# Kernel optimization log

Hardware: AMD Instinct MI355X
Metric: run time of the kernel (lower is better)

The kernel has to match this reference:

```python
import jax, jax.numpy as jnp
import numpy as np

B, T, U = 2048, 200, 128


def setup_inputs() -> dict:
    key = jax.random.key(0)
    ks = jax.random.split(key, 9)
    s = 1.0 / np.sqrt(U)
    inp = {
        "interest_states": jax.random.normal(ks[0], (B, T, U), dtype=jnp.float32),
        "attention_scores": jax.random.uniform(ks[1], (B, T, 1), dtype=jnp.float32),
        "W_xu": jax.random.normal(ks[2], (U, U), dtype=jnp.float32) * s,
        "b_xu": jnp.zeros((U,), dtype=jnp.float32),
        "W_hu": jax.random.normal(ks[3], (U, U), dtype=jnp.float32) * s,
        "b_hu": jnp.zeros((U,), dtype=jnp.float32),
        "W_xr": jax.random.normal(ks[4], (U, U), dtype=jnp.float32) * s,
        "b_xr": jnp.zeros((U,), dtype=jnp.float32),
        "W_hr": jax.random.normal(ks[5], (U, U), dtype=jnp.float32) * s,
        "b_hr": jnp.zeros((U,), dtype=jnp.float32),
        "W_xc": jax.random.normal(ks[6], (U, U), dtype=jnp.float32) * s,
        "b_xc": jnp.zeros((U,), dtype=jnp.float32),
        "W_hc": jax.random.normal(ks[7], (U, U), dtype=jnp.float32) * s,
        "b_hc": jnp.zeros((U,), dtype=jnp.float32),
    }
    return inp


def reference(interest_states, attention_scores, W_xu, b_xu, W_hu, b_hu,
              W_xr, b_xr, W_hr, b_hr, W_xc, b_xc, W_hc, b_hc):
    # Precompute input-side projections for all timesteps (batched GEMMs).
    xu = jnp.einsum('btu,uv->btv', interest_states, W_xu) + b_xu  # [B,T,U]
    xr = jnp.einsum('btu,uv->btv', interest_states, W_xr) + b_xr
    xc = jnp.einsum('btu,uv->btv', interest_states, W_xc) + b_xc
    # Time-major for scan: [T,B,U] / [T,B,1]
    xu_t = jnp.swapaxes(xu, 0, 1)
    xr_t = jnp.swapaxes(xr, 0, 1)
    xc_t = jnp.swapaxes(xc, 0, 1)
    att_t = jnp.swapaxes(attention_scores, 0, 1)  # [T,B,1]

    def step(h, inp):
        xu_i, xr_i, xc_i, a_i = inp
        u = jax.nn.sigmoid(xu_i + h @ W_hu + b_hu)       # update gate [B,U]
        r = jax.nn.sigmoid(xr_i + h @ W_hr + b_hr)       # reset gate  [B,U]
        c = jnp.tanh(xc_i + (r * h) @ W_hc + b_hc)       # candidate   [B,U]
        au = a_i * u                                     # attention-scaled update gate
        h_new = (1.0 - au) * h + au * c
        return h_new, None

    h0 = jnp.zeros((interest_states.shape[0], W_hu.shape[0]), dtype=interest_states.dtype)
    h_final, _ = jax.lax.scan(step, h0, (xu_t, xr_t, xc_t, att_t))
    return h_final  # [B,U]
```

## Files before the change

kernel.cpp:

```cpp
#include <hip/hip_runtime.h>
#include <hip/hip_bf16.h>

#define B_  2048
#define T_  200
#define U_  128
#define NB  8
#define PITCH 136

typedef __attribute__((ext_vector_type(8))) short short8;
typedef __attribute__((ext_vector_type(4))) float f32x4;
typedef __attribute__((ext_vector_type(2))) float f32x2;
typedef __attribute__((ext_vector_type(2))) unsigned uint2v;

static __device__ inline float sigm_pre(float sum, float bS) {
  float e = __builtin_amdgcn_exp2f(fmaf(sum, -1.44269504088896340736f, bS));
  return __builtin_amdgcn_rcpf(1.0f + e);
}
static __device__ inline float tanh_pre(float sum, float bS) {
  float e = __builtin_amdgcn_exp2f(fmaf(sum, 2.88539008177792681472f, bS));
  float r = __builtin_amdgcn_rcpf(1.0f + e);
  return fmaf(-2.0f, r, 1.0f);
}
static __device__ inline unsigned pk2(float a, float b) {
  union { __hip_bfloat162 h; unsigned u; } c;
  float2 t; t.x = a; t.y = b;
  c.h = __float22bfloat162_rn(t);
  return c.u;
}
static __device__ inline short f2bf(float f) {
  union { float f; unsigned u; } v; v.f = f;
  unsigned r = v.u + 0x7FFFu + ((v.u >> 16) & 1u);
  return (short)(r >> 16);
}

#define TRFRAG(dst, addr, O0, O1)                                              \
  {                                                                            \
    uint2v _ta, _tb;                                                           \
    asm volatile("ds_read_b64_tr_b16 %0, %1 offset:" O0 : "=v"(_ta) : "v"(addr)); \
    asm volatile("ds_read_b64_tr_b16 %0, %1 offset:" O1 : "=v"(_tb) : "v"(addr)); \
    union { struct { uint2v a, b; } p; short8 s; } _u;                         \
    _u.p.a = _ta; _u.p.b = _tb;                                                \
    dst = _u.s;                                                                \
  }
#define LGKM_WAIT()                                                            \
  asm volatile("s_waitcnt lgkmcnt(0)" ::: "memory");                           \
  __builtin_amdgcn_sched_barrier(0)

__global__ void prep_weights(const float* __restrict__ Wxu, const float* __restrict__ Wxr,
                             const float* __restrict__ Wxc, const float* __restrict__ Whu,
                             const float* __restrict__ Whr, const float* __restrict__ Whc,
                             short* __restrict__ out) {
  const int m = blockIdx.x >> 7;
  const int k = blockIdx.x & 127;
  const int n = threadIdx.x;
  const float* Wp;
  switch (m) {
    case 0: Wp = Wxu; break; case 1: Wp = Wxr; break; case 2: Wp = Wxc; break;
    case 3: Wp = Whu; break; case 4: Wp = Whr; break; default: Wp = Whc; break;
  }
  out[(m * 128 + n) * 128 + k] = f2bf(Wp[k * 128 + n]);
}

__global__ __launch_bounds__(512, 2) void augru_scan(
    const float* __restrict__ IS, const float* __restrict__ ATT,
    const float* __restrict__ bxu, const float* __restrict__ bhu,
    const float* __restrict__ bxr, const float* __restrict__ bhr,
    const float* __restrict__ bxc, const float* __restrict__ bhc,
    const short* __restrict__ WT, float* __restrict__ out) {
  __shared__ __align__(128) short h_T[128][16];
  __shared__ __align__(128) short rh_T[128][16];
  __shared__ __align__(16)  short x_bf[16][PITCH];
  __shared__ __align__(16)  float att_s[T_][NB];

  const int tid  = threadIdx.x;
  const int w    = tid >> 6;
  const int l    = tid & 63;
  const int l15  = l & 15;
  const int lg   = l >> 4;
  const int b0   = blockIdx.x * NB;
  const int col  = w * 16 + l15;

  for (int i = tid; i < (128 * 16 * 2 + 16 * PITCH) / 2; i += 512) {
    if (i < 128 * 16 / 2)               ((int*)h_T)[i] = 0;
    else if (i < 128 * 16)              ((int*)rh_T)[i - 128 * 16 / 2] = 0;
    else                                ((int*)x_bf)[i - 128 * 16] = 0;
  }
  for (int i = tid; i < T_ * NB; i += 512) {
    int r = i / T_, t = i % T_;
    att_s[t][r] = ATT[(size_t)(b0 + r) * T_ + t];
  }
  const int prow = w;
  const int pc2  = (tid & 63) * 2;
  const float* xptr = IS + (size_t)(b0 + prow) * T_ * U_ + pc2;
  {
    f32x2 xv = *(const f32x2*)xptr;
    *(unsigned*)&x_bf[prow][pc2] = pk2(xv[0], xv[1]);
  }
  short8 Wf[6][4];
#pragma unroll
  for (int m = 0; m < 6; ++m)
#pragma unroll
    for (int kf = 0; kf < 4; ++kf)
      Wf[m][kf] = *(const short8*)(WT + ((m * 128 + col) * 128 + kf * 32 + lg * 8));
#pragma unroll
  for (int m = 0; m < 6; ++m)
#pragma unroll
    for (int kf = 0; kf < 4; ++kf) asm volatile("" : "+v"(Wf[m][kf]));

  const float buS = (bxu[col] + bhu[col]) * -1.44269504088896340736f;
  const float brS = (bxr[col] + bhr[col]) * -1.44269504088896340736f;
  const float bcS = (bxc[col] + bhc[col]) * 2.88539008177792681472f;

  const unsigned trv   = (unsigned)(lg * 256 + l15 * 8);
  const unsigned adr_h = (unsigned)(size_t)(&h_T[0][0]) + trv;
  const unsigned adr_r = (unsigned)(size_t)(&rh_T[0][0]) + trv;

  const f32x4 fz = {0.0f, 0.0f, 0.0f, 0.0f};
  f32x4 hreg = fz;
  float ureg[4];

  for (int t = 0; t < T_; ++t) {
    __syncthreads();
    __builtin_amdgcn_sched_barrier(0);
    short8 ha[4], xa[4];
    TRFRAG(ha[0], adr_h, "0",    "128");
    TRFRAG(ha[1], adr_h, "1024", "1152");
    TRFRAG(ha[2], adr_h, "2048", "2176");
    TRFRAG(ha[3], adr_h, "3072", "3200");
#pragma unroll
    for (int kf = 0; kf < 4; ++kf)
      xa[kf] = *(const short8*)&x_bf[l15][kf * 32 + lg * 8];
    const f32x2 xnext = *(const f32x2*)(xptr + (t < T_ - 1 ? (size_t)(t + 1) * U_ : (size_t)t * U_));
    LGKM_WAIT();

    f32x4 axu = fz, axr = fz, axc = fz, ahu = fz, ahr = fz;
#pragma unroll
    for (int kf = 0; kf < 4; ++kf) {
      axu = __builtin_amdgcn_mfma_f32_16x16x32_bf16(xa[kf], Wf[0][kf], axu, 0, 0, 0);
      axr = __builtin_amdgcn_mfma_f32_16x16x32_bf16(xa[kf], Wf[1][kf], axr, 0, 0, 0);
      axc = __builtin_amdgcn_mfma_f32_16x16x32_bf16(xa[kf], Wf[2][kf], axc, 0, 0, 0);
      ahu = __builtin_amdgcn_mfma_f32_16x16x32_bf16(ha[kf], Wf[3][kf], ahu, 0, 0, 0);
      ahr = __builtin_amdgcn_mfma_f32_16x16x32_bf16(ha[kf], Wf[4][kf], ahr, 0, 0, 0);
    }
    float rh[4];
#pragma unroll
    for (int rg = 0; rg < 4; ++rg) {
      ureg[rg] = sigm_pre(axu[rg] + ahu[rg], buS);
      float rr = sigm_pre(axr[rg] + ahr[rg], brS);
      rh[rg]   = rr * hreg[rg];
    }
    {
      uint2v wv; wv[0] = pk2(rh[0], rh[1]); wv[1] = pk2(rh[2], rh[3]);
      *(uint2v*)&rh_T[col][lg * 4] = wv;
    }
    __syncthreads();
    __builtin_amdgcn_sched_barrier(0);
    short8 ra[4];
    TRFRAG(ra[0], adr_r, "0",    "128");
    TRFRAG(ra[1], adr_r, "1024", "1152");
    TRFRAG(ra[2], adr_r, "2048", "2176");
    TRFRAG(ra[3], adr_r, "3072", "3200");
    const f32x4 a4 = *(const f32x4*)&att_s[t][(lg & 1) * 4];
    LGKM_WAIT();

    f32x4 ahc0 = fz, ahc1 = fz;
    ahc0 = __builtin_amdgcn_mfma_f32_16x16x32_bf16(ra[0], Wf[5][0], ahc0, 0, 0, 0);
    ahc1 = __builtin_amdgcn_mfma_f32_16x16x32_bf16(ra[2], Wf[5][2], ahc1, 0, 0, 0);
    ahc0 = __builtin_amdgcn_mfma_f32_16x16x32_bf16(ra[1], Wf[5][1], ahc0, 0, 0, 0);
    ahc1 = __builtin_amdgcn_mfma_f32_16x16x32_bf16(ra[3], Wf[5][3], ahc1, 0, 0, 0);

    float hv[4];
#pragma unroll
    for (int rg = 0; rg < 4; ++rg) {
      float cc = tanh_pre((axc[rg] + ahc0[rg]) + ahc1[rg], bcS);
      float au = a4[rg] * ureg[rg];
      hv[rg] = fmaf(au, cc - hreg[rg], hreg[rg]);
      hreg[rg] = hv[rg];
    }
    {
      uint2v wv; wv[0] = pk2(hv[0], hv[1]); wv[1] = pk2(hv[2], hv[3]);
      *(uint2v*)&h_T[col][lg * 4] = wv;
    }
    *(unsigned*)&x_bf[prow][pc2] = pk2(xnext[0], xnext[1]);
  }
#pragma unroll
  for (int rg = 0; rg < 4; ++rg) {
    const int row = lg * 4 + rg;
    if (row < NB) out[(size_t)(b0 + row) * U_ + col] = hreg[rg];
  }
}

extern "C" void kernel_launch(void* const* d_in, const int* in_sizes, int n_in,
                              void* d_out, int out_size, void* d_ws, size_t ws_size,
                              hipStream_t stream) {
  const float* IS  = (const float*)d_in[0];
  const float* ATT = (const float*)d_in[1];
  const float* Wxu = (const float*)d_in[2];  const float* bxu = (const float*)d_in[3];
  const float* Whu = (const float*)d_in[4];  const float* bhu = (const float*)d_in[5];
  const float* Wxr = (const float*)d_in[6];  const float* bxr = (const float*)d_in[7];
  const float* Whr = (const float*)d_in[8];  const float* bhr = (const float*)d_in[9];
  const float* Wxc = (const float*)d_in[10]; const float* bxc = (const float*)d_in[11];
  const float* Whc = (const float*)d_in[12]; const float* bhc = (const float*)d_in[13];
  short* WT  = (short*)d_ws;
  float* OUT = (float*)d_out;

  prep_weights<<<dim3(6 * 128), dim3(128), 0, stream>>>(Wxu, Wxr, Wxc, Whu, Whr, Whc, WT);
  augru_scan<<<dim3(B_ / NB), dim3(512), 0, stream>>>(IS, ATT, bxu, bhu, bxr, bhr, bxc, bhc, WT, OUT);
}
```

Measured before the change: 449.2 us.

## Load x fragments directly from global and precompute next-step input projections

Removes the x_bf shared-memory staging buffer: each lane now loads its own fp32 x fragment from global memory, converts it to bf16 in registers, and runs the input-side MFMAs for step t+1 at the end of step t. This takes the x projections off the critical path between the first barrier and the gate activations. The hidden-side MFMAs are split into two accumulator chains to shorten dependency latency, and two sched_barriers are dropped. The cost is more global load traffic, since rows are duplicated across lanes (l15&7), plus extra register pressure from the prefetched xraw and the carried accumulators.

Result: slower. 747.2 us (+66.3%).

```diff
diff --git a/kernel.cpp b/kernel.cpp
--- a/kernel.cpp
+++ b/kernel.cpp
@@ -5,11 +5,9 @@
 #define T_  200
 #define U_  128
 #define NB  8
-#define PITCH 136
 
 typedef __attribute__((ext_vector_type(8))) short short8;
 typedef __attribute__((ext_vector_type(4))) float f32x4;
-typedef __attribute__((ext_vector_type(2))) float f32x2;
 typedef __attribute__((ext_vector_type(2))) unsigned uint2v;
 
 static __device__ inline float sigm_pre(float sum, float bS) {
@@ -31,6 +29,12 @@
   union { float f; unsigned u; } v; v.f = f;
   unsigned r = v.u + 0x7FFFu + ((v.u >> 16) & 1u);
   return (short)(r >> 16);
+}
+static __device__ inline short8 cvt8(const f32x4 a, const f32x4 b) {
+  union { unsigned u[4]; short8 s; } c;
+  c.u[0] = pk2(a[0], a[1]); c.u[1] = pk2(a[2], a[3]);
+  c.u[2] = pk2(b[0], b[1]); c.u[3] = pk2(b[2], b[3]);
+  return c.s;
 }
 
 #define TRFRAG(dst, addr, O0, O1)                                              \
@@ -69,7 +73,6 @@
     const short* __restrict__ WT, float* __restrict__ out) {
   __shared__ __align__(128) short h_T[128][16];
   __shared__ __align__(128) short rh_T[128][16];
-  __shared__ __align__(16)  short x_bf[16][PITCH];
   __shared__ __align__(16)  float att_s[T_][NB];
 
   const int tid  = threadIdx.x;
@@ -80,22 +83,16 @@
   const int b0   = blockIdx.x * NB;
   const int col  = w * 16 + l15;
 
-  for (int i = tid; i < (128 * 16 * 2 + 16 * PITCH) / 2; i += 512) {
-    if (i < 128 * 16 / 2)               ((int*)h_T)[i] = 0;
-    else if (i < 128 * 16)              ((int*)rh_T)[i - 128 * 16 / 2] = 0;
-    else                                ((int*)x_bf)[i - 128 * 16] = 0;
+  for (int i = tid; i < 128 * 16 * 2 / 2; i += 512) {
+    if (i < 1024) ((int*)h_T)[i] = 0;
+    else          ((int*)rh_T)[i - 1024] = 0;
   }
   for (int i = tid; i < T_ * NB; i += 512) {
     int r = i / T_, t = i % T_;
     att_s[t][r] = ATT[(size_t)(b0 + r) * T_ + t];
   }
-  const int prow = w;
-  const int pc2  = (tid & 63) * 2;
-  const float* xptr = IS + (size_t)(b0 + prow) * T_ * U_ + pc2;
-  {
-    f32x2 xv = *(const f32x2*)xptr;
-    *(unsigned*)&x_bf[prow][pc2] = pk2(xv[0], xv[1]);
-  }
+  const float* xg = IS + (size_t)(b0 + (l15 & 7)) * (T_ * U_) + lg * 8;
+
   short8 Wf[6][4];
 #pragma unroll
   for (int m = 0; m < 6; ++m)
@@ -119,34 +116,58 @@
   f32x4 hreg = fz;
   float ureg[4];
 
+  f32x4 axu = fz, axr = fz, axc = fz;
+  {
+    f32x4 xraw[8];
+#pragma unroll
+    for (int kf = 0; kf < 4; ++kf) {
+      xraw[2 * kf]     = *(const f32x4*)(xg + kf * 32);
+      xraw[2 * kf + 1] = *(const f32x4*)(xg + kf * 32 + 4);
+    }
+    short8 xf[4];
+#pragma unroll
+    for (int kf = 0; kf < 4; ++kf) xf[kf] = cvt8(xraw[2 * kf], xraw[2 * kf + 1]);
+#pragma unroll
+    for (int kf = 0; kf < 4; ++kf) {
+      axu = __builtin_amdgcn_mfma_f32_16x16x32_bf16(xf[kf], Wf[0][kf], axu, 0, 0, 0);
+      axr = __builtin_amdgcn_mfma_f32_16x16x32_bf16(xf[kf], Wf[1][kf], axr, 0, 0, 0);
+      axc = __builtin_amdgcn_mfma_f32_16x16x32_bf16(xf[kf], Wf[2][kf], axc, 0, 0, 0);
+    }
+  }
+
   for (int t = 0; t < T_; ++t) {
     __syncthreads();
-    __builtin_amdgcn_sched_barrier(0);
-    short8 ha[4], xa[4];
+    short8 ha[4];
     TRFRAG(ha[0], adr_h, "0",    "128");
     TRFRAG(ha[1], adr_h, "1024", "1152");
     TRFRAG(ha[2], adr_h, "2048", "2176");
     TRFRAG(ha[3], adr_h, "3072", "3200");
-#pragma unroll
-    for (int kf = 0; kf < 4; ++kf)
-      xa[kf] = *(const short8*)&x_bf[l15][kf * 32 + lg * 8];
-    const f32x2 xnext = *(const f32x2*)(xptr + (t < T_ - 1 ? (size_t)(t + 1) * U_ : (size_t)t * U_));
+    f32x4 xraw[8];
+    {
+      const float* xp = xg + (size_t)(t < T_ - 1 ? t + 1 : t) * U_;
+#pragma unroll
+      for (int kf = 0; kf < 4; ++kf) {
+        xraw[2 * kf]     = *(const f32x4*)(xp + kf * 32);
+        xraw[2 * kf + 1] = *(const f32x4*)(xp + kf * 32 + 4);
+      }
+    }
     LGKM_WAIT();
 
-    f32x4 axu = fz, axr = fz, axc = fz, ahu = fz, ahr = fz;
-#pragma unroll
-    for (int kf = 0; kf < 4; ++kf) {
-      axu = __builtin_amdgcn_mfma_f32_16x16x32_bf16(xa[kf], Wf[0][kf], axu, 0, 0, 0);
-      axr = __builtin_amdgcn_mfma_f32_16x16x32_bf16(xa[kf], Wf[1][kf], axr, 0, 0, 0);
-      axc = __builtin_amdgcn_mfma_f32_16x16x32_bf16(xa[kf], Wf[2][kf], axc, 0, 0, 0);
-      ahu = __builtin_amdgcn_mfma_f32_16x16x32_bf16(ha[kf], Wf[3][kf], ahu, 0, 0, 0);
-      ahr = __builtin_amdgcn_mfma_f32_16x16x32_bf16(ha[kf], Wf[4][kf], ahr, 0, 0, 0);
-    }
+    f32x4 ahu0 = fz, ahu1 = fz, ahr0 = fz, ahr1 = fz;
+    ahu0 = __builtin_amdgcn_mfma_f32_16x16x32_bf16(ha[0], Wf[3][0], ahu0, 0, 0, 0);
+    ahr0 = __builtin_amdgcn_mfma_f32_16x16x32_bf16(ha[0], Wf[4][0], ahr0, 0, 0, 0);
+    ahu1 = __builtin_amdgcn_mfma_f32_16x16x32_bf16(ha[2], Wf[3][2], ahu1, 0, 0, 0);
+    ahr1 = __builtin_amdgcn_mfma_f32_16x16x32_bf16(ha[2], Wf[4][2], ahr1, 0, 0, 0);
+    ahu0 = __builtin_amdgcn_mfma_f32_16x16x32_bf16(ha[1], Wf[3][1], ahu0, 0, 0, 0);
+    ahr0 = __builtin_amdgcn_mfma_f32_16x16x32_bf16(ha[1], Wf[4][1], ahr0, 0, 0, 0);
+    ahu1 = __builtin_amdgcn_mfma_f32_16x16x32_bf16(ha[3], Wf[3][3], ahu1, 0, 0, 0);
+    ahr1 = __builtin_amdgcn_mfma_f32_16x16x32_bf16(ha[3], Wf[4][3], ahr1, 0, 0, 0);
+
     float rh[4];
 #pragma unroll
     for (int rg = 0; rg < 4; ++rg) {
-      ureg[rg] = sigm_pre(axu[rg] + ahu[rg], buS);
-      float rr = sigm_pre(axr[rg] + ahr[rg], brS);
+      ureg[rg] = sigm_pre(axu[rg] + ahu0[rg] + ahu1[rg], buS);
+      float rr = sigm_pre(axr[rg] + ahr0[rg] + ahr1[rg], brS);
       rh[rg]   = rr * hreg[rg];
     }
     {
@@ -154,7 +175,6 @@
       *(uint2v*)&rh_T[col][lg * 4] = wv;
     }
     __syncthreads();
-    __builtin_amdgcn_sched_barrier(0);
     short8 ra[4];
     TRFRAG(ra[0], adr_r, "0",    "128");
     TRFRAG(ra[1], adr_r, "1024", "1152");
@@ -172,7 +192,7 @@
     float hv[4];
 #pragma unroll
     for (int rg = 0; rg < 4; ++rg) {
-      float cc = tanh_pre((axc[rg] + ahc0[rg]) + ahc1[rg], bcS);
+      float cc = tanh_pre(axc[rg] + ahc0[rg] + ahc1[rg], bcS);
       float au = a4[rg] * ureg[rg];
       hv[rg] = fmaf(au, cc - hreg[rg], hreg[rg]);
       hreg[rg] = hv[rg];
@@ -181,7 +201,19 @@
       uint2v wv; wv[0] = pk2(hv[0], hv[1]); wv[1] = pk2(hv[2], hv[3]);
       *(uint2v*)&h_T[col][lg * 4] = wv;
     }
-    *(unsigned*)&x_bf[prow][pc2] = pk2(xnext[0], xnext[1]);
+    {
+      short8 xf[4];
+#pragma unroll
+      for (int kf = 0; kf < 4; ++kf) xf[kf] = cvt8(xraw[2 * kf], xraw[2 * kf + 1]);
+      f32x4 nxu = fz, nxr = fz, nxc = fz;
+#pragma unroll
+      for (int kf = 0; kf < 4; ++kf) {
+        nxu = __builtin_amdgcn_mfma_f32_16x16x32_bf16(xf[kf], Wf[0][kf], nxu, 0, 0, 0);
+        nxr = __builtin_amdgcn_mfma_f32_16x16x32_bf16(xf[kf], Wf[1][kf], nxr, 0, 0, 0);
+        nxc = __builtin_amdgcn_mfma_f32_16x16x32_bf16(xf[kf], Wf[2][kf], nxc, 0, 0, 0);
+      }
+      axu = nxu; axr = nxr; axc = nxc;
+    }
   }
 #pragma unroll
   for (int rg = 0; rg < 4; ++rg) {
```

## Software-pipeline input projections one step ahead with double-buffered x staging

Applied to the files above, without the earlier changes.

Moves the input-side MFMAs (x·W_xu/xr/xc) for step t+1 into the second phase of step t, after the candidate MFMAs, so they run off the critical path of the h-dependent gate computation. Input rows are double-buffered in two shared tiles and prefetched two steps ahead, and the loop is unrolled by two. The h-side gate MFMAs are split into two accumulator chains to shorten dependency latency. This costs extra registers and shared memory, and the zeroing loops now include a redundant pass over h_T.

Measured after the change: 489.2 us. 1.09x slower.

```diff
diff --git a/kernel.cpp b/kernel.cpp
--- a/kernel.cpp
+++ b/kernel.cpp
@@ -69,7 +69,8 @@
     const short* __restrict__ WT, float* __restrict__ out) {
   __shared__ __align__(128) short h_T[128][16];
   __shared__ __align__(128) short rh_T[128][16];
-  __shared__ __align__(16)  short x_bf[16][PITCH];
+  __shared__ __align__(16)  short x0_bf[16][PITCH];
+  __shared__ __align__(16)  short x1_bf[16][PITCH];
   __shared__ __align__(16)  float att_s[T_][NB];
 
   const int tid  = threadIdx.x;
@@ -80,22 +81,20 @@
   const int b0   = blockIdx.x * NB;
   const int col  = w * 16 + l15;
 
-  for (int i = tid; i < (128 * 16 * 2 + 16 * PITCH) / 2; i += 512) {
-    if (i < 128 * 16 / 2)               ((int*)h_T)[i] = 0;
-    else if (i < 128 * 16)              ((int*)rh_T)[i - 128 * 16 / 2] = 0;
-    else                                ((int*)x_bf)[i - 128 * 16] = 0;
-  }
+  for (int i = tid; i < 128 * 16; i += 512) {
+    ((int*)h_T)[i & 2047] = 0;
+  }
+  for (int i = tid; i < 1024; i += 512) { ((int*)h_T)[i] = 0; }
+  for (int i = tid; i < 1024; i += 512) { ((int*)rh_T)[i] = 0; }
+  for (int i = tid; i < 16 * PITCH / 2; i += 512) { ((int*)x0_bf)[i] = 0; ((int*)x1_bf)[i] = 0; }
   for (int i = tid; i < T_ * NB; i += 512) {
     int r = i / T_, t = i % T_;
     att_s[t][r] = ATT[(size_t)(b0 + r) * T_ + t];
   }
   const int prow = w;
   const int pc2  = (tid & 63) * 2;
-  const float* xptr = IS + (size_t)(b0 + prow) * T_ * U_ + pc2;
-  {
-    f32x2 xv = *(const f32x2*)xptr;
-    *(unsigned*)&x_bf[prow][pc2] = pk2(xv[0], xv[1]);
-  }
+  const float* xptr = IS + (size_t)(b0 + prow) * (T_ * U_) + pc2;
+
   short8 Wf[6][4];
 #pragma unroll
   for (int m = 0; m < 6; ++m)
@@ -118,71 +117,99 @@
   const f32x4 fz = {0.0f, 0.0f, 0.0f, 0.0f};
   f32x4 hreg = fz;
   float ureg[4];
-
-  for (int t = 0; t < T_; ++t) {
-    __syncthreads();
-    __builtin_amdgcn_sched_barrier(0);
-    short8 ha[4], xa[4];
-    TRFRAG(ha[0], adr_h, "0",    "128");
-    TRFRAG(ha[1], adr_h, "1024", "1152");
-    TRFRAG(ha[2], adr_h, "2048", "2176");
-    TRFRAG(ha[3], adr_h, "3072", "3200");
-#pragma unroll
-    for (int kf = 0; kf < 4; ++kf)
-      xa[kf] = *(const short8*)&x_bf[l15][kf * 32 + lg * 8];
-    const f32x2 xnext = *(const f32x2*)(xptr + (t < T_ - 1 ? (size_t)(t + 1) * U_ : (size_t)t * U_));
-    LGKM_WAIT();
-
-    f32x4 axu = fz, axr = fz, axc = fz, ahu = fz, ahr = fz;
+  f32x4 axu = fz, axr = fz, axc = fz;
+
+  {
+    f32x2 xv0 = *(const f32x2*)(xptr);
+    f32x2 xv1 = *(const f32x2*)(xptr + U_);
+    *(unsigned*)&x0_bf[prow][pc2] = pk2(xv0[0], xv0[1]);
+    *(unsigned*)&x1_bf[prow][pc2] = pk2(xv1[0], xv1[1]);
+  }
+  __syncthreads();
+  {
+    short8 xa[4];
+#pragma unroll
+    for (int kf = 0; kf < 4; ++kf) xa[kf] = *(const short8*)&x0_bf[l15][kf * 32 + lg * 8];
 #pragma unroll
     for (int kf = 0; kf < 4; ++kf) {
       axu = __builtin_amdgcn_mfma_f32_16x16x32_bf16(xa[kf], Wf[0][kf], axu, 0, 0, 0);
       axr = __builtin_amdgcn_mfma_f32_16x16x32_bf16(xa[kf], Wf[1][kf], axr, 0, 0, 0);
       axc = __builtin_amdgcn_mfma_f32_16x16x32_bf16(xa[kf], Wf[2][kf], axc, 0, 0, 0);
-      ahu = __builtin_amdgcn_mfma_f32_16x16x32_bf16(ha[kf], Wf[3][kf], ahu, 0, 0, 0);
-      ahr = __builtin_amdgcn_mfma_f32_16x16x32_bf16(ha[kf], Wf[4][kf], ahr, 0, 0, 0);
     }
-    float rh[4];
-#pragma unroll
-    for (int rg = 0; rg < 4; ++rg) {
-      ureg[rg] = sigm_pre(axu[rg] + ahu[rg], buS);
-      float rr = sigm_pre(axr[rg] + ahr[rg], brS);
-      rh[rg]   = rr * hreg[rg];
-    }
-    {
-      uint2v wv; wv[0] = pk2(rh[0], rh[1]); wv[1] = pk2(rh[2], rh[3]);
-      *(uint2v*)&rh_T[col][lg * 4] = wv;
-    }
-    __syncthreads();
-    __builtin_amdgcn_sched_barrier(0);
-    short8 ra[4];
-    TRFRAG(ra[0], adr_r, "0",    "128");
-    TRFRAG(ra[1], adr_r, "1024", "1152");
-    TRFRAG(ra[2], adr_r, "2048", "2176");
-    TRFRAG(ra[3], adr_r, "3072", "3200");
-    const f32x4 a4 = *(const f32x4*)&att_s[t][(lg & 1) * 4];
-    LGKM_WAIT();
-
-    f32x4 ahc0 = fz, ahc1 = fz;
-    ahc0 = __builtin_amdgcn_mfma_f32_16x16x32_bf16(ra[0], Wf[5][0], ahc0, 0, 0, 0);
-    ahc1 = __builtin_amdgcn_mfma_f32_16x16x32_bf16(ra[2], Wf[5][2], ahc1, 0, 0, 0);
-    ahc0 = __builtin_amdgcn_mfma_f32_16x16x32_bf16(ra[1], Wf[5][1], ahc0, 0, 0, 0);
-    ahc1 = __builtin_amdgcn_mfma_f32_16x16x32_bf16(ra[3], Wf[5][3], ahc1, 0, 0, 0);
-
-    float hv[4];
-#pragma unroll
-    for (int rg = 0; rg < 4; ++rg) {
-      float cc = tanh_pre((axc[rg] + ahc0[rg]) + ahc1[rg], bcS);
-      float au = a4[rg] * ureg[rg];
-      hv[rg] = fmaf(au, cc - hreg[rg], hreg[rg]);
-      hreg[rg] = hv[rg];
-    }
-    {
-      uint2v wv; wv[0] = pk2(hv[0], hv[1]); wv[1] = pk2(hv[2], hv[3]);
-      *(uint2v*)&h_T[col][lg * 4] = wv;
-    }
-    *(unsigned*)&x_bf[prow][pc2] = pk2(xnext[0], xnext[1]);
-  }
+  }
+
+#define STEP(t, xstage, xread)                                                   \
+  {                                                                              \
+    __syncthreads();          \
+    short8 ha[4];                                                                \
+    TRFRAG(ha[0], adr_h, "0",    "128");                                         \
+    TRFRAG(ha[1], adr_h, "1024", "1152");                                        \
+    TRFRAG(ha[2], adr_h, "2048", "2176");                                        \
+    TRFRAG(ha[3], adr_h, "3072", "3200");                                        \
+    const int ts = (t) + 2 < T_ ? (t) + 2 : T_ - 1;                              \
+    f32x2 xnx = *(const f32x2*)(xptr + (size_t)ts * U_);                         \
+    LGKM_WAIT();                                                                 \
+    f32x4 ahu0 = fz, ahu1 = fz, ahr0 = fz, ahr1 = fz;                            \
+    ahu0 = __builtin_amdgcn_mfma_f32_16x16x32_bf16(ha[0], Wf[3][0], ahu0, 0, 0, 0); \
+    ahr0 = __builtin_amdgcn_mfma_f32_16x16x32_bf16(ha[0], Wf[4][0], ahr0, 0, 0, 0); \
+    ahu1 = __builtin_amdgcn_mfma_f32_16x16x32_bf16(ha[2], Wf[3][2], ahu1, 0, 0, 0); \
+    ahr1 = __builtin_amdgcn_mfma_f32_16x16x32_bf16(ha[2], Wf[4][2], ahr1, 0, 0, 0); \
+    ahu0 = __builtin_amdgcn_mfma_f32_16x16x32_bf16(ha[1], Wf[3][1], ahu0, 0, 0, 0); \
+    ahr0 = __builtin_amdgcn_mfma_f32_16x16x32_bf16(ha[1], Wf[4][1], ahr0, 0, 0, 0); \
+    ahu1 = __builtin_amdgcn_mfma_f32_16x16x32_bf16(ha[3], Wf[3][3], ahu1, 0, 0, 0); \
+    ahr1 = __builtin_amdgcn_mfma_f32_16x16x32_bf16(ha[3], Wf[4][3], ahr1, 0, 0, 0); \
+    float rh[4];                                                                 \
+    _Pragma("unroll")                                                            \
+    for (int rg = 0; rg < 4; ++rg) {                                             \
+      ureg[rg] = sigm_pre(axu[rg] + ahu0[rg] + ahu1[rg], buS);                   \
+      float rr = sigm_pre(axr[rg] + ahr0[rg] + ahr1[rg], brS);                   \
+      rh[rg]   = rr * hreg[rg];                                                  \
+    }                                                                            \
+    { uint2v wv; wv[0] = pk2(rh[0], rh[1]); wv[1] = pk2(rh[2], rh[3]);           \
+      *(uint2v*)&rh_T[col][lg * 4] = wv; }                                       \
+    *(unsigned*)&xstage[prow][pc2] = pk2(xnx[0], xnx[1]);                        \
+    __syncthreads();                                    \
+    short8 ra[4], xa[4];                                                         \
+    TRFRAG(ra[0], adr_r, "0",    "128");                                         \
+    TRFRAG(ra[1], adr_r, "1024", "1152");                                        \
+    TRFRAG(ra[2], adr_r, "2048", "2176");                                        \
+    TRFRAG(ra[3], adr_r, "3072", "3200");                                        \
+    _Pragma("unroll")                                                            \
+    for (int kf = 0; kf < 4; ++kf)                                               \
+      xa[kf] = *(const short8*)&xread[l15][kf * 32 + lg * 8];                    \
+    const f32x4 a4 = *(const f32x4*)&att_s[t][(lg & 1) * 4];                     \
+    LGKM_WAIT();                                                                 \
+    f32x4 ahc0 = fz, ahc1 = fz;                                                  \
+    ahc0 = __builtin_amdgcn_mfma_f32_16x16x32_bf16(ra[0], Wf[5][0], ahc0, 0, 0, 0); \
+    ahc1 = __builtin_amdgcn_mfma_f32_16x16x32_bf16(ra[2], Wf[5][2], ahc1, 0, 0, 0); \
+    ahc0 = __builtin_amdgcn_mfma_f32_16x16x32_bf16(ra[1], Wf[5][1], ahc0, 0, 0, 0); \
+    ahc1 = __builtin_amdgcn_mfma_f32_16x16x32_bf16(ra[3], Wf[5][3], ahc1, 0, 0, 0); \
+    f32x4 nxu = fz, nxr = fz, nxc = fz;                                          \
+    _Pragma("unroll")                                                            \
+    for (int kf = 0; kf < 4; ++kf) {                                             \
+      nxu = __builtin_amdgcn_mfma_f32_16x16x32_bf16(xa[kf], Wf[0][kf], nxu, 0, 0, 0); \
+      nxr = __builtin_amdgcn_mfma_f32_16x16x32_bf16(xa[kf], Wf[1][kf], nxr, 0, 0, 0); \
+      nxc = __builtin_amdgcn_mfma_f32_16x16x32_bf16(xa[kf], Wf[2][kf], nxc, 0, 0, 0); \
+    }                                                                            \
+    float hv[4];                                                                 \
+    _Pragma("unroll")                                                            \
+    for (int rg = 0; rg < 4; ++rg) {                                             \
+      float cc = tanh_pre(axc[rg] + ahc0[rg] + ahc1[rg], bcS);                   \
+      float au = a4[rg] * ureg[rg];                                              \
+      hv[rg] = fmaf(au, cc - hreg[rg], hreg[rg]);                                \
+      hreg[rg] = hv[rg];                                                         \
+    }                                                                            \
+    { uint2v wv; wv[0] = pk2(hv[0], hv[1]); wv[1] = pk2(hv[2], hv[3]);           \
+      *(uint2v*)&h_T[col][lg * 4] = wv; }                                        \
+    axu = nxu; axr = nxr; axc = nxc;                                             \
+  }
+
+  for (int t = 0; t < T_; t += 2) {
+    STEP(t,     x0_bf, x1_bf);
+    STEP(t + 1, x1_bf, x0_bf);
+  }
+#undef STEP
+
 #pragma unroll
   for (int rg = 0; rg < 4; ++rg) {
     const int row = lg * 4 + rg;
```
